# Kernel tuning notes

Hardware: AMD Instinct MI355X
Metric: run time of the kernel (lower is better)

Reference implementation:

```python
import jax, jax.numpy as jnp
import numpy as np

K = 3; STRIDE = 1; PAD = 1; DIL = 1; DG = 1  # deformable_groups = 1


def _conv2d(x, w, b, stride, pad):
    out = jax.lax.conv_general_dilated(
        x, w, (stride, stride), [(pad, pad), (pad, pad)],
        dimension_numbers=("NCHW", "OIHW", "NCHW"))
    return out + b[None, :, None, None]


def setup_inputs() -> dict:
    key = jax.random.key(0)
    k1, k2, k3 = jax.random.split(key, 3)
    B, Cin, H, W = 4, 64, 160, 160
    Cout = 64
    inp = {
        "input": jax.random.normal(k1, (B, Cin, H, W), dtype=jnp.float32),
        # offset/mask conv: dg*3*k*k = 27 output channels; scaled small so offsets are O(few px)
        "w_off": jax.random.normal(k2, (DG * 3 * K * K, Cin, K, K), dtype=jnp.float32) * 0.1,
        "b_off": jnp.zeros((DG * 3 * K * K,), dtype=jnp.float32),
        "w_dcn": jax.random.normal(k3, (Cout, Cin, K, K), dtype=jnp.float32) * 0.05,
        "b_dcn": jnp.zeros((Cout,), dtype=jnp.float32),
    }
    return inp


def _dcnv2(x, offset, mask, w, b):
    # x: [B,C,H,W]; offset: [B,2*kk,Ho,Wo]; mask: [B,kk,Ho,Wo] (already sigmoided)
    B, C, H, W = x.shape
    kk = K * K
    Ho, Wo = offset.shape[2], offset.shape[3]
    # mmcv channel layout within a deformable group: channel 2*p = y-offset, 2*p+1 = x-offset
    off = offset.reshape(B, kk, 2, Ho, Wo)
    off_y, off_x = off[:, :, 0], off[:, :, 1]            # [B,kk,Ho,Wo]

    ki, kj = jnp.meshgrid(jnp.arange(K), jnp.arange(K), indexing="ij")
    ki = ki.reshape(kk).astype(jnp.float32)
    kj = kj.reshape(kk).astype(jnp.float32)
    hs = (jnp.arange(Ho) * STRIDE - PAD).astype(jnp.float32)
    ws = (jnp.arange(Wo) * STRIDE - PAD).astype(jnp.float32)
    base_y = hs[None, :, None] + (ki * DIL)[:, None, None]   # [kk,Ho,1]
    base_x = ws[None, None, :] + (kj * DIL)[:, None, None]   # [kk,1,Wo]

    y = base_y[None] + off_y   # [B,kk,Ho,Wo]
    xx = base_x[None] + off_x

    y0 = jnp.floor(y); x0 = jnp.floor(xx)
    dy = y - y0; dx = xx - x0
    y0i = y0.astype(jnp.int32); y1i = y0i + 1
    x0i = x0.astype(jnp.int32); x1i = x0i + 1

    def gather(img, yi, xi):
        # img [C,H,W]; yi/xi [kk,Ho,Wo]; zero padding outside the image
        valid = (yi >= 0) & (yi < H) & (xi >= 0) & (xi < W)
        yc = jnp.clip(yi, 0, H - 1)
        xc = jnp.clip(xi, 0, W - 1)
        return img[:, yc, xc] * valid[None]   # [C,kk,Ho,Wo]

    gb = jax.vmap(gather)
    g00 = gb(x, y0i, x0i)
    g01 = gb(x, y0i, x1i)
    g10 = gb(x, y1i, x0i)
    g11 = gb(x, y1i, x1i)

    w00 = ((1 - dy) * (1 - dx))[:, None]   # [B,1,kk,Ho,Wo]
    w01 = ((1 - dy) * dx)[:, None]
    w10 = (dy * (1 - dx))[:, None]
    w11 = (dy * dx)[:, None]
    val = g00 * w00 + g01 * w01 + g10 * w10 + g11 * w11   # [B,C,kk,Ho,Wo]

    val = val * mask[:, None]                              # modulation
    Cout = w.shape[0]
    out = jnp.einsum("bckhw,ock->bohw", val, w.reshape(Cout, C, kk))
    return out + b[None, :, None, None]


def reference(input, w_off, b_off, w_dcn, b_dcn):
    om = _conv2d(input, w_off, b_off, STRIDE, PAD)   # [B, 3*kk, Ho, Wo]
    o1, o2, mask = jnp.split(om, 3, axis=1)
    offset = jnp.concatenate([o1, o2], axis=1)
    mask = jax.nn.sigmoid(mask)
    return _dcnv2(input, offset, mask, w_dcn, b_dcn)
```

## Files before the change

### kernel.cpp

```cpp
#include <hip/hip_runtime.h>
#include <math.h>

#define B_   4
#define CIN  64
#define H_   160
#define W_   160
#define COUT 64
#define OFFC 27
#define HW_  (H_ * W_)
#define NPIX (B_ * HW_)

#define TILE_P 128
#define VPITCH 130


__global__ __launch_bounds__(256) void k_transpose_nhwc(const float* __restrict__ in,
                                                        float* __restrict__ out) {
    __shared__ float tile[CIN][33];
    int blk = blockIdx.x;
    int wc  = blk % 5;
    int by  = blk / 5;
    int y   = by % H_;
    int b   = by / H_;
    int w0  = wc * 32;
    int t   = threadIdx.x;

    int wi = t & 31, ch = t >> 5;
#pragma unroll
    for (int r = 0; r < 8; ++r) {
        int c = r * 8 + ch;
        tile[c][wi] = in[((b * CIN + c) * H_ + y) * W_ + w0 + wi];
    }
    __syncthreads();
    int c2 = t & 63, wj = t >> 6;
#pragma unroll
    for (int r = 0; r < 8; ++r) {
        int wi2 = r * 4 + wj;
        out[((b * H_ + y) * W_ + w0 + wi2) * CIN + c2] = tile[c2][wi2];
    }
}

__global__ void k_transpose_w(const float* __restrict__ w, float* __restrict__ wT) {
    int i  = blockIdx.x * 256 + threadIdx.x;
    int co = i & 63;
    int kc = i >> 6;
    int c  = kc & 63;
    int k  = kc >> 6;
    wT[i] = w[(co * CIN + c) * 9 + k];
}

__global__ __launch_bounds__(256, 4) void k_offconv(const float* __restrict__ in,
                                                    const float* __restrict__ wo,
                                                    const float* __restrict__ bo,
                                                    float* __restrict__ om2) {
    int bid = (int)blockIdx.x;
    int id  = (bid & 7) * 150 + (bid >> 3);
    int g   = id % 3;
    int pb  = id / 3;
    int p   = pb * 256 + threadIdx.x;
    int b   = p / HW_;
    int rem = p - b * HW_;
    int y   = rem / W_;
    int x   = rem - y * W_;

    int   off[9];
    float valid[9];
#pragma unroll
    for (int di = 0; di < 3; ++di) {
        int yy = y + di - 1;
        int yc = min(max(yy, 0), H_ - 1);
        bool yok = (yy >= 0) & (yy < H_);
#pragma unroll
        for (int dj = 0; dj < 3; ++dj) {
            int xx = x + dj - 1;
            int xc = min(max(xx, 0), W_ - 1);
            bool ok = yok & (xx >= 0) & (xx < W_);
            off[di * 3 + dj]   = yc * W_ + xc;
            valid[di * 3 + dj] = ok ? 1.f : 0.f;
        }
    }

    float acc[9];
#pragma unroll
    for (int j = 0; j < 9; ++j) acc[j] = bo[g * 9 + j];

    const float* inb = in + (size_t)b * CIN * HW_;
    const float* wg  = wo + (size_t)(g * 9) * 576;
#pragma unroll 2
    for (int c = 0; c < CIN; ++c) {
        float v[9];
#pragma unroll
        for (int tp = 0; tp < 9; ++tp)
            v[tp] = inb[c * HW_ + off[tp]] * valid[tp];
#pragma unroll
        for (int j = 0; j < 9; ++j) {
#pragma unroll
            for (int tp = 0; tp < 9; ++tp)
                acc[j] += v[tp] * wg[j * 576 + c * 9 + tp];
        }
    }
#pragma unroll
    for (int j = 0; j < 9; ++j)
        om2[(size_t)(g * 9 + j) * NPIX + p] = acc[j];
}

template <bool NHWC>
__global__ __launch_bounds__(256, 4) void k_dcn(const float* __restrict__ xsrc,
                                                const float* __restrict__ om2,
                                                const float* __restrict__ wT,
                                                const float* __restrict__ bd,
                                                float* __restrict__ out) {
    __shared__ __align__(16) float sk[TILE_P * 8];
    __shared__ __align__(16) float vals[64 * VPITCH];

    int t   = threadIdx.x;
    int bid = (int)blockIdx.x;
    int blk = (bid & 7) * ((NPIX / TILE_P) / 8) + (bid >> 3);
    int p0  = blk * TILE_P;
    int b   = p0 / HW_;
    int rb  = p0 - b * HW_;

    int lane = t & 63;
    int co0  = __builtin_amdgcn_readfirstlane((t >> 6) << 4);

    float acc[2][16];
#pragma unroll
    for (int j = 0; j < 16; ++j) {
        float bj = bd[co0 + j];
        acc[0][j] = bj;
        acc[1][j] = bj;
    }

    const float* base = xsrc + (size_t)b * CIN * HW_;

    for (int k = 0; k < 9; ++k) {
        __syncthreads();

        if (t < TILE_P) {
            int pix = t;
            int p   = p0 + pix;
            int rem = rb + pix;
            int y   = rem / W_;
            int x   = rem - y * W_;
            float oy = om2[(size_t)(2 * k) * NPIX + p];
            float ox = om2[(size_t)(2 * k + 1) * NPIX + p];
            float mr = om2[(size_t)(18 + k) * NPIX + p];
            float m  = 1.f / (1.f + expf(-mr));
            int ki = k / 3, kj = k - ki * 3;
            float fy  = (float)(y - 1 + ki) + oy;
            float fx  = (float)(x - 1 + kj) + ox;
            float fy0 = floorf(fy), fx0 = floorf(fx);
            float dy = fy - fy0, dx = fx - fx0;
            int iy = (int)fy0, ix = (int)fx0;
            bool yok0 = (iy >= 0) & (iy < H_);
            bool yok1 = (iy + 1 >= 0) & (iy + 1 < H_);
            bool xok0 = (ix >= 0) & (ix < W_);
            bool xok1 = (ix + 1 >= 0) & (ix + 1 < W_);
            int iyc0 = min(max(iy, 0), H_ - 1);
            int iyc1 = min(max(iy + 1, 0), H_ - 1);
            int ixc0 = min(max(ix, 0), W_ - 1);
            int ixc1 = min(max(ix + 1, 0), W_ - 1);
            const int mul = NHWC ? 64 : 1;
            float4 swt, sof;
            swt.x = (1.f - dy) * (1.f - dx) * m * (float)(yok0 & xok0);
            swt.y = (1.f - dy) * dx         * m * (float)(yok0 & xok1);
            swt.z = dy * (1.f - dx)         * m * (float)(yok1 & xok0);
            swt.w = dy * dx                 * m * (float)(yok1 & xok1);
            sof.x = __int_as_float((iyc0 * W_ + ixc0) * mul);
            sof.y = __int_as_float((iyc0 * W_ + ixc1) * mul);
            sof.z = __int_as_float((iyc1 * W_ + ixc0) * mul);
            sof.w = __int_as_float((iyc1 * W_ + ixc1) * mul);
            *reinterpret_cast<float4*>(sk + pix * 8)     = swt;
            *reinterpret_cast<float4*>(sk + pix * 8 + 4) = sof;
        }
        __syncthreads();

        if constexpr (NHWC) {
#pragma unroll 4
            for (int it = 0; it < 16; ++it) {
                int i     = t + it * 256;
                int cpair = i & 31;
                int c0    = cpair * 2;
                int pix   = i >> 5;
                const float* s = sk + pix * 8;
                float4 sw = *reinterpret_cast<const float4*>(s);
                float4 so = *reinterpret_cast<const float4*>(s + 4);
                float2 g00 = *reinterpret_cast<const float2*>(base + __float_as_int(so.x) + c0);
                float2 g01 = *reinterpret_cast<const float2*>(base + __float_as_int(so.y) + c0);
                float2 g10 = *reinterpret_cast<const float2*>(base + __float_as_int(so.z) + c0);
                float2 g11 = *reinterpret_cast<const float2*>(base + __float_as_int(so.w) + c0);
                vals[c0 * VPITCH + pix]       = g00.x * sw.x + g01.x * sw.y + g10.x * sw.z + g11.x * sw.w;
                vals[(c0 + 1) * VPITCH + pix] = g00.y * sw.x + g01.y * sw.y + g10.y * sw.z + g11.y * sw.w;
            }
        } else {
            int cbase = (t & 63) * HW_;
#pragma unroll 4
            for (int it = 0; it < 32; ++it) {
                int i   = t + it * 256;
                int c   = i & 63;
                int pix = i >> 6;
                const float* s = sk + pix * 8;
                float4 sw = *reinterpret_cast<const float4*>(s);
                float4 so = *reinterpret_cast<const float4*>(s + 4);
                float g00 = base[__float_as_int(so.x) + cbase];
                float g01 = base[__float_as_int(so.y) + cbase];
                float g10 = base[__float_as_int(so.z) + cbase];
                float g11 = base[__float_as_int(so.w) + cbase];
                vals[c * VPITCH + pix] = g00 * sw.x + g01 * sw.y + g10 * sw.z + g11 * sw.w;
            }
        }
        __syncthreads();

        const float* wk = wT + (k * 64) * 64 + co0;
#pragma unroll 4
        for (int c = 0; c < 64; ++c) {
            float2 v = *reinterpret_cast<const float2*>(vals + c * VPITCH + 2 * lane);
            const float* wp = wk + c * 64;
            float4 wv0 = *reinterpret_cast<const float4*>(wp);
            float4 wv1 = *reinterpret_cast<const float4*>(wp + 4);
            float4 wv2 = *reinterpret_cast<const float4*>(wp + 8);
            float4 wv3 = *reinterpret_cast<const float4*>(wp + 12);
            float wr[16] = {wv0.x, wv0.y, wv0.z, wv0.w,
                            wv1.x, wv1.y, wv1.z, wv1.w,
                            wv2.x, wv2.y, wv2.z, wv2.w,
                            wv3.x, wv3.y, wv3.z, wv3.w};
#pragma unroll
            for (int j = 0; j < 16; ++j) {
                acc[0][j] += v.x * wr[j];
                acc[1][j] += v.y * wr[j];
            }
        }
    }

    __syncthreads();
#pragma unroll
    for (int j = 0; j < 16; ++j) {
        float2 o2;
        o2.x = acc[0][j];
        o2.y = acc[1][j];
        *reinterpret_cast<float2*>(vals + (co0 + j) * VPITCH + 2 * lane) = o2;
    }
    __syncthreads();
#pragma unroll 4
    for (int it = 0; it < 32; ++it) {
        int i   = t + it * 256;
        int co  = i >> 7;
        int pix = i & 127;
        out[((size_t)(b * COUT + co)) * HW_ + rb + pix] = vals[co * VPITCH + pix];
    }
}

extern "C" void kernel_launch(void* const* d_in, const int* in_sizes, int n_in,
                              void* d_out, int out_size, void* d_ws, size_t ws_size,
                              hipStream_t stream) {
    const float* input = (const float*)d_in[0];
    const float* w_off = (const float*)d_in[1];
    const float* b_off = (const float*)d_in[2];
    const float* w_dcn = (const float*)d_in[3];
    const float* b_dcn = (const float*)d_in[4];
    float* out = (float*)d_out;

    const size_t XN_F = (size_t)NPIX * CIN;
    const size_t OM_F = (size_t)NPIX * OFFC;
    const size_t WT_F = 576 * 64;
    const size_t need_full = (XN_F + OM_F + WT_F) * sizeof(float);

    float* ws = (float*)d_ws;
    if (ws_size >= need_full) {
        float* x_nhwc = ws;
        float* om2    = ws + XN_F;
        float* wT     = om2 + OM_F;
        k_transpose_nhwc<<<dim3(B_ * H_ * 5), dim3(256), 0, stream>>>(input, x_nhwc);
        k_transpose_w<<<dim3(144), dim3(256), 0, stream>>>(w_dcn, wT);
        k_offconv<<<dim3(1200), dim3(256), 0, stream>>>(input, w_off, b_off, om2);
        k_dcn<true><<<dim3(NPIX / TILE_P), dim3(256), 0, stream>>>(x_nhwc, om2, wT, b_dcn, out);
    } else {
        float* om2 = ws;
        float* wT  = om2 + OM_F;
        k_transpose_w<<<dim3(144), dim3(256), 0, stream>>>(w_dcn, wT);
        k_offconv<<<dim3(1200), dim3(256), 0, stream>>>(input, w_off, b_off, om2);
        k_dcn<false><<<dim3(NPIX / TILE_P), dim3(256), 0, stream>>>(input, om2, wT, b_dcn, out);
    }
}
```

Before: 328.4 us.

## Halve DCN pixel tile to raise occupancy and unroll offset conv by channel pairs

The deformable-conv kernel's pixel tile drops from 128 to 64, so each thread keeps 16 accumulators instead of 32 and the launch bound goes from 4 to 6 blocks per SIMD. The bilinear gather is restructured so each lane owns one channel and wavefronts step across pixels, merging the NHWC and NCHW paths. The offset conv's channel loop is manually unrolled by two. Smaller tiles cost more weight reloads and more blocks in exchange for lower register pressure and shared memory use.

```diff
diff --git a/kernel.cpp b/kernel.cpp
--- a/kernel.cpp
+++ b/kernel.cpp
@@ -10,8 +10,8 @@
 #define HW_  (H_ * W_)
 #define NPIX (B_ * HW_)
 
-#define TILE_P 128
-#define VPITCH 130
+#define TILE_P 64
+#define VP2    65
 
 
 __global__ __launch_bounds__(256) void k_transpose_nhwc(const float* __restrict__ in,
@@ -86,17 +86,22 @@
 
     const float* inb = in + (size_t)b * CIN * HW_;
     const float* wg  = wo + (size_t)(g * 9) * 576;
-#pragma unroll 2
-    for (int c = 0; c < CIN; ++c) {
-        float v[9];
+    for (int c = 0; c < CIN; c += 2) {
+        float va[9], vb[9];
 #pragma unroll
         for (int tp = 0; tp < 9; ++tp)
-            v[tp] = inb[c * HW_ + off[tp]] * valid[tp];
+            va[tp] = inb[c * HW_ + off[tp]] * valid[tp];
+#pragma unroll
+        for (int tp = 0; tp < 9; ++tp)
+            vb[tp] = inb[(c + 1) * HW_ + off[tp]] * valid[tp];
 #pragma unroll
         for (int j = 0; j < 9; ++j) {
 #pragma unroll
             for (int tp = 0; tp < 9; ++tp)
-                acc[j] += v[tp] * wg[j * 576 + c * 9 + tp];
+                acc[j] += va[tp] * wg[j * 576 + c * 9 + tp];
+#pragma unroll
+            for (int tp = 0; tp < 9; ++tp)
+                acc[j] += vb[tp] * wg[j * 576 + (c + 1) * 9 + tp];
         }
     }
 #pragma unroll
@@ -105,13 +110,13 @@
 }
 
 template <bool NHWC>
-__global__ __launch_bounds__(256, 4) void k_dcn(const float* __restrict__ xsrc,
+__global__ __launch_bounds__(256, 6) void k_dcn(const float* __restrict__ xsrc,
                                                 const float* __restrict__ om2,
                                                 const float* __restrict__ wT,
                                                 const float* __restrict__ bd,
                                                 float* __restrict__ out) {
     __shared__ __align__(16) float sk[TILE_P * 8];
-    __shared__ __align__(16) float vals[64 * VPITCH];
+    __shared__ __align__(16) float vals[64 * VP2];
 
     int t   = threadIdx.x;
     int bid = (int)blockIdx.x;
@@ -123,13 +128,9 @@
     int lane = t & 63;
     int co0  = __builtin_amdgcn_readfirstlane((t >> 6) << 4);
 
-    float acc[2][16];
-#pragma unroll
-    for (int j = 0; j < 16; ++j) {
-        float bj = bd[co0 + j];
-        acc[0][j] = bj;
-        acc[1][j] = bj;
-    }
+    float acc[16];
+#pragma unroll
+    for (int j = 0; j < 16; ++j) acc[j] = bd[co0 + j];
 
     const float* base = xsrc + (size_t)b * CIN * HW_;
 
@@ -137,9 +138,8 @@
         __syncthreads();
 
         if (t < TILE_P) {
-            int pix = t;
-            int p   = p0 + pix;
-            int rem = rb + pix;
+            int p   = p0 + t;
+            int rem = rb + t;
             int y   = rem / W_;
             int x   = rem - y * W_;
             float oy = om2[(size_t)(2 * k) * NPIX + p];
@@ -170,43 +170,25 @@
             sof.y = __int_as_float((iyc0 * W_ + ixc1) * mul);
             sof.z = __int_as_float((iyc1 * W_ + ixc0) * mul);
             sof.w = __int_as_float((iyc1 * W_ + ixc1) * mul);
-            *reinterpret_cast<float4*>(sk + pix * 8)     = swt;
-            *reinterpret_cast<float4*>(sk + pix * 8 + 4) = sof;
+            *reinterpret_cast<float4*>(sk + t * 8)     = swt;
+            *reinterpret_cast<float4*>(sk + t * 8 + 4) = sof;
         }
         __syncthreads();
 
-        if constexpr (NHWC) {
+        {
+            int c     = lane;
+            int cterm = NHWC ? c : c * HW_;
 #pragma unroll 4
             for (int it = 0; it < 16; ++it) {
-                int i     = t + it * 256;
-                int cpair = i & 31;
-                int c0    = cpair * 2;
-                int pix   = i >> 5;
+                int pix = (t >> 6) + 4 * it;
                 const float* s = sk + pix * 8;
                 float4 sw = *reinterpret_cast<const float4*>(s);
                 float4 so = *reinterpret_cast<const float4*>(s + 4);
-                float2 g00 = *reinterpret_cast<const float2*>(base + __float_as_int(so.x) + c0);
-                float2 g01 = *reinterpret_cast<const float2*>(base + __float_as_int(so.y) + c0);
-                float2 g10 = *reinterpret_cast<const float2*>(base + __float_as_int(so.z) + c0);
-                float2 g11 = *reinterpret_cast<const float2*>(base + __float_as_int(so.w) + c0);
-                vals[c0 * VPITCH + pix]       = g00.x * sw.x + g01.x * sw.y + g10.x * sw.z + g11.x * sw.w;
-                vals[(c0 + 1) * VPITCH + pix] = g00.y * sw.x + g01.y * sw.y + g10.y * sw.z + g11.y * sw.w;
-            }
-        } else {
-            int cbase = (t & 63) * HW_;
-#pragma unroll 4
-            for (int it = 0; it < 32; ++it) {
-                int i   = t + it * 256;
-                int c   = i & 63;
-                int pix = i >> 6;
-                const float* s = sk + pix * 8;
-                float4 sw = *reinterpret_cast<const float4*>(s);
-                float4 so = *reinterpret_cast<const float4*>(s + 4);
-                float g00 = base[__float_as_int(so.x) + cbase];
-                float g01 = base[__float_as_int(so.y) + cbase];
-                float g10 = base[__float_as_int(so.z) + cbase];
-                float g11 = base[__float_as_int(so.w) + cbase];
-                vals[c * VPITCH + pix] = g00 * sw.x + g01 * sw.y + g10 * sw.z + g11 * sw.w;
+                float g00 = base[__float_as_int(so.x) + cterm];
+                float g01 = base[__float_as_int(so.y) + cterm];
+                float g10 = base[__float_as_int(so.z) + cterm];
+                float g11 = base[__float_as_int(so.w) + cterm];
+                vals[c * VP2 + pix] = g00 * sw.x + g01 * sw.y + g10 * sw.z + g11 * sw.w;
             }
         }
         __syncthreads();
@@ -214,39 +196,34 @@
         const float* wk = wT + (k * 64) * 64 + co0;
 #pragma unroll 4
         for (int c = 0; c < 64; ++c) {
-            float2 v = *reinterpret_cast<const float2*>(vals + c * VPITCH + 2 * lane);
+            float v = vals[c * VP2 + lane];
             const float* wp = wk + c * 64;
             float4 wv0 = *reinterpret_cast<const float4*>(wp);
             float4 wv1 = *reinterpret_cast<const float4*>(wp + 4);
             float4 wv2 = *reinterpret_cast<const float4*>(wp + 8);
             float4 wv3 = *reinterpret_cast<const float4*>(wp + 12);
-            float wr[16] = {wv0.x, wv0.y, wv0.z, wv0.w,
-                            wv1.x, wv1.y, wv1.z, wv1.w,
-                            wv2.x, wv2.y, wv2.z, wv2.w,
-                            wv3.x, wv3.y, wv3.z, wv3.w};
-#pragma unroll
-            for (int j = 0; j < 16; ++j) {
-                acc[0][j] += v.x * wr[j];
-                acc[1][j] += v.y * wr[j];
-            }
+            acc[0]  += v * wv0.x;  acc[1]  += v * wv0.y;
+            acc[2]  += v * wv0.z;  acc[3]  += v * wv0.w;
+            acc[4]  += v * wv1.x;  acc[5]  += v * wv1.y;
+            acc[6]  += v * wv1.z;  acc[7]  += v * wv1.w;
+            acc[8]  += v * wv2.x;  acc[9]  += v * wv2.y;
+            acc[10] += v * wv2.z;  acc[11] += v * wv2.w;
+            acc[12] += v * wv3.x;  acc[13] += v * wv3.y;
+            acc[14] += v * wv3.z;  acc[15] += v * wv3.w;
         }
     }
 
     __syncthreads();
 #pragma unroll
-    for (int j = 0; j < 16; ++j) {
-        float2 o2;
-        o2.x = acc[0][j];
-        o2.y = acc[1][j];
-        *reinterpret_cast<float2*>(vals + (co0 + j) * VPITCH + 2 * lane) = o2;
-    }
+    for (int j = 0; j < 16; ++j)
+        vals[(co0 + j) * VP2 + lane] = acc[j];
     __syncthreads();
 #pragma unroll 4
-    for (int it = 0; it < 32; ++it) {
-        int i   = t + it * 256;
-        int co  = i >> 7;
-        int pix = i & 127;
-        out[((size_t)(b * COUT + co)) * HW_ + rb + pix] = vals[co * VPITCH + pix];
+    for (int it = 0; it < 16; ++it) {
+        int i  = t + it * 256;
+        int co = i >> 6;
+        int px = i & 63;
+        out[((size_t)(b * COUT + co)) * HW_ + rb + px] = vals[co * VP2 + px];
     }
 }
 
```

Result: faster. 319.9 us (-2.6%).
